# Kernel tuning notes

Hardware: AMD Instinct MI355X
Metric: run time of the kernel (lower is better)

## Reference

```python
import jax, jax.numpy as jnp
import numpy as np
from jax import lax

B, N, D = 16, 2048, 256
H = 64  # hidden_dim
EPS = 1e-5


def zero_softmax(x, eps=EPS):
    # zeros stay exactly zero: exp(0)-1 == 0
    e = jnp.exp(x) - 1.0
    return e / (jnp.sum(e, axis=-1, keepdims=True) + eps)


def setup_inputs() -> dict:
    key = jax.random.key(0)
    ks = jax.random.split(key, 9)
    s_in = 1.0 / np.sqrt(D)
    x = jax.random.normal(ks[0], (B, N, D), dtype=jnp.float32)
    Wq = jax.random.uniform(ks[1], (D, H), jnp.float32, -s_in, s_in)
    bq = jax.random.uniform(ks[2], (H,), jnp.float32, -s_in, s_in)
    Wk = jax.random.uniform(ks[3], (D, H), jnp.float32, -s_in, s_in)
    bk = jax.random.uniform(ks[4], (H,), jnp.float32, -s_in, s_in)
    Wv = jax.random.uniform(ks[5], (D, H), jnp.float32, -s_in, s_in)
    bv = jax.random.uniform(ks[6], (H,), jnp.float32, -s_in, s_in)
    s_c = 1.0 / 3.0  # conv fan_in = 1*3*3 = 9
    conv_w = jax.random.uniform(ks[7], (1, 1, 3, 3), jnp.float32, -s_c, s_c)
    conv_b = jax.random.uniform(ks[8], (1,), jnp.float32, -s_c, s_c)
    return {"x": x, "Wq": Wq, "bq": bq, "Wk": Wk, "bk": bk,
            "Wv": Wv, "bv": bv, "conv_w": conv_w, "conv_b": conv_b}


def reference(x, Wq, bq, Wk, bk, Wv, bv, conv_w, conv_b):
    scale = H ** (-0.5)
    q = jnp.einsum('bnd,dh->bnh', x, Wq) + bq
    k = jnp.einsum('bnd,dh->bnh', x, Wk) + bk
    v = jnp.einsum('bnd,dh->bnh', x, Wv) + bv
    A_dense = jnp.einsum('bnh,bmh->bnm', q, k) * scale  # [B, N, N]
    A_in = A_dense[:, None, :, :]  # [B, 1, N, N]
    A_conv = lax.conv_general_dilated(
        A_in, conv_w, window_strides=(1, 1), padding='SAME',
        dimension_numbers=('NCHW', 'OIHW', 'NCHW')) + conv_b[None, :, None, None]
    A_conv = jax.nn.sigmoid(A_conv)[:, 0, :, :]
    A_sparse = jax.nn.relu(A_dense - A_conv)
    A_norm = zero_softmax(A_sparse)
    return jnp.einsum('bnm,bmh->bnh', A_norm, v)
```

## Files before the change

kernel.cpp:

```cpp
#include <hip/hip_runtime.h>
#include <hip/hip_bf16.h>

typedef __bf16 bf16_t;
typedef __bf16 bf16x8 __attribute__((ext_vector_type(8)));
typedef float  floatx4 __attribute__((ext_vector_type(4)));

#define BQ 16
#define NTOK 2048
#define DIM 256
#define HD 64

__global__ __launch_bounds__(256) void k_prep(const float* __restrict__ Wq,
                                              const float* __restrict__ Wk,
                                              const float* __restrict__ Wv,
                                              bf16_t* __restrict__ wt,
                                              float* __restrict__ outz,
                                              float* __restrict__ rsz) {
    int o = blockIdx.x * 256 + threadIdx.x;
    if (o < 49152) {
        int w = o >> 14;
        int r = o & 16383;
        int h = r >> 8;
        int d = r & 255;
        const float* W = (w == 0) ? Wq : ((w == 1) ? Wk : Wv);
        wt[o] = (bf16_t)W[d * 64 + h];
    }
    float4 z = make_float4(0.f, 0.f, 0.f, 0.f);
    for (int u = o; u < 532480; u += 262144) {
        if (u < 524288) ((float4*)outz)[u] = z;
        else            ((float4*)rsz)[u - 524288] = z;
    }
}

#define XS 264
__global__ __launch_bounds__(256) void k_qkv(const float* __restrict__ x,
                                             const bf16_t* __restrict__ wt,
                                             const float* __restrict__ bq,
                                             const float* __restrict__ bk,
                                             const float* __restrict__ bv,
                                             bf16_t* __restrict__ qb,
                                             bf16_t* __restrict__ kb,
                                             bf16_t* __restrict__ vt) {
    __shared__ bf16_t x_ls[64 * XS];
    __shared__ bf16_t vt_ls[64 * 72];

    int b  = blockIdx.x >> 5;
    int t0 = (blockIdx.x & 31) << 6;
    int t  = threadIdx.x;
    int lane = t & 63;
    int w    = t >> 6;
    int m_   = lane & 15;
    int q4   = lane >> 4;

    const bf16_t* wrow = wt + (16 * w + m_) * 256 + q4 * 8;

    bf16x8 bfr[2][3];
    #pragma unroll
    for (int wi = 0; wi < 3; ++wi)
        bfr[0][wi] = *(const bf16x8*)(wrow + wi * 16384);

    for (int tau = t; tau < 4096; tau += 256) {
        int row = tau >> 6, ch = tau & 63;
        float4 v = ((const float4*)x)[(size_t)(b * NTOK + t0 + row) * 64 + ch];
        bf16_t tmp[4] = {(bf16_t)v.x, (bf16_t)v.y, (bf16_t)v.z, (bf16_t)v.w};
        *(uint2*)(&x_ls[row * XS + ch * 4]) = *(uint2*)tmp;
    }
    __syncthreads();

    floatx4 acc[3][4];
    #pragma unroll
    for (int wi = 0; wi < 3; ++wi)
        #pragma unroll
        for (int mt = 0; mt < 4; ++mt) acc[wi][mt] = floatx4{0.f, 0.f, 0.f, 0.f};

    #pragma unroll
    for (int ks = 0; ks < 8; ++ks) {
        if (ks < 7) {
            #pragma unroll
            for (int wi = 0; wi < 3; ++wi)
                bfr[(ks + 1) & 1][wi] = *(const bf16x8*)(wrow + wi * 16384 + (ks + 1) * 32);
        }
        #pragma unroll
        for (int mt = 0; mt < 4; ++mt) {
            bf16x8 afrag = *(const bf16x8*)(&x_ls[(16 * mt + m_) * XS + ks * 32 + q4 * 8]);
            #pragma unroll
            for (int wi = 0; wi < 3; ++wi)
                acc[wi][mt] = __builtin_amdgcn_mfma_f32_16x16x32_bf16(afrag, bfr[ks & 1][wi], acc[wi][mt], 0, 0, 0);
        }
    }

    float biasq = bq[16 * w + m_];
    float biask = bk[16 * w + m_];
    float biasv = bv[16 * w + m_];

    #pragma unroll
    for (int mt = 0; mt < 4; ++mt)
        #pragma unroll
        for (int r = 0; r < 4; ++r) {
            int tok = t0 + 16 * mt + 4 * q4 + r;
            qb[(size_t)(b * NTOK + tok) * 64 + 16 * w + m_] = (bf16_t)((acc[0][mt][r] + biasq) * 0.125f);
            kb[(size_t)(b * NTOK + tok) * 64 + 16 * w + m_] = (bf16_t)(acc[1][mt][r] + biask);
            vt_ls[(16 * w + m_) * 72 + 16 * mt + 4 * q4 + r] = (bf16_t)(acc[2][mt][r] + biasv);
        }
    __syncthreads();
    for (int tau = t; tau < 512; tau += 256) {
        int h = tau >> 3, ch = tau & 7;
        uint4 val = *(const uint4*)(&vt_ls[h * 72 + ch * 8]);
        *(uint4*)(vt + (size_t)(b * 64 + h) * NTOK + t0 + ch * 8) = val;
    }
}

#define SP 72
#define RINT 62
#define L2E 1.44269504f

static __device__ __forceinline__ bf16x8 as_bf16x8(uint4 u) {
    union { uint4 a; bf16x8 b; } c; c.a = u; return c.b;
}

__global__ __launch_bounds__(512, 3) void k_attn(const bf16_t* __restrict__ qb,
                                                 const bf16_t* __restrict__ kb,
                                                 const bf16_t* __restrict__ vt,
                                                 const float* __restrict__ conv_w,
                                                 const float* __restrict__ conv_b,
                                                 float* __restrict__ outp,
                                                 float* __restrict__ rsg) {
    __shared__ bf16_t k_ls[64 * SP];
    __shared__ bf16_t v_ls[64 * SP];
    __shared__ bf16_t a_bf[64 * SP];
    __shared__ bf16_t p_raw[64 * SP + 8];
    bf16_t* pv_ls = p_raw + 8;

    int b  = blockIdx.z;
    int r0 = blockIdx.x * RINT;
    int cy = blockIdx.y;
    int it_beg = (cy * 34) / 3;
    int it_end = ((cy + 1) * 34) / 3;

    int t = threadIdx.x, lane = t & 63, w = t >> 6;
    int m_ = lane & 15, q4 = lane >> 4;
    int wtj = w & 3;
    int wti = (w >> 2) << 1;

    const uint* vt32 = (const uint*)vt + (size_t)b * 64 * 1024;
    const bf16_t* kb_b = kb + (size_t)b * NTOK * 64;

    int krow = t >> 3, kch = t & 7;

    uint4 kreg;
    uint  vreg[4];
    auto load_k = [&](int c0) {
        int g = c0 - 1 + krow;
        uint4 val = make_uint4(0u, 0u, 0u, 0u);
        if (g >= 0 && g < NTOK)
            val = *(const uint4*)(kb_b + (size_t)g * 64 + kch * 8);
        kreg = val;
    };
    auto load_v = [&](int c0) {
        int cb2 = (c0 >> 1) + 4 * kch;
        #pragma unroll
        for (int j = 0; j < 4; ++j) {
            uint val = 0u;
            if (cb2 + j < 1024) val = vt32[krow * 1024 + cb2 + j];
            vreg[j] = val;
        }
    };

    load_k(it_beg * RINT);
    load_v(it_beg * RINT);

    float cw9[9];
    #pragma unroll
    for (int i = 0; i < 9; ++i) cw9[i] = conv_w[i] * L2E;
    float cbv2 = conv_b[0] * L2E;
    int koff = ((wtj & 1) << 3) + ((wtj & 2) * 12);
    bf16x8 bK[3];
    #pragma unroll
    for (int di = 0; di < 3; ++di) {
        bf16_t tmp[8];
        #pragma unroll
        for (int jj = 0; jj < 8; ++jj) {
            int d = koff + q4 * 8 + jj - (16 * wtj + m_) + 1;
            tmp[jj] = (bf16_t)((d >= 0 && d < 3) ? cw9[3 * di + d] : 0.f);
        }
        bK[di] = *(bf16x8*)tmp;
    }

    bf16x8 qreg[2][2];
    #pragma unroll
    for (int p = 0; p < 2; ++p) {
        int g = r0 - 1 + 16 * (wti + p) + m_;
        #pragma unroll
        for (int ks = 0; ks < 2; ++ks) {
            uint4 val = make_uint4(0u, 0u, 0u, 0u);
            if (g >= 0 && g < NTOK)
                val = *(const uint4*)(qb + (size_t)(b * NTOK + g) * 64 + ks * 32 + q4 * 8);
            qreg[p][ks] = as_bf16x8(val);
        }
    }

    for (int u = t; u < 2308; u += 512) ((uint*)p_raw)[u] = 0u;

    *(uint4*)(&k_ls[krow * SP + kch * 8]) = kreg;
    load_k((it_beg + 1) * RINT);

    floatx4 accO[2], rsacc[2];
    accO[0] = floatx4{0.f, 0.f, 0.f, 0.f};
    accO[1] = floatx4{0.f, 0.f, 0.f, 0.f};
    rsacc[0] = floatx4{0.f, 0.f, 0.f, 0.f};
    rsacc[1] = floatx4{0.f, 0.f, 0.f, 0.f};

    float mj = ((wtj == 0 && m_ == 0) || (wtj == 3 && m_ == 15)) ? 0.f : 1.f;
    int jm1 = 16 * wtj + m_ - 1;

    __syncthreads();

    for (int itg = it_beg; itg < it_end; ++itg) {
        floatx4 areg[2];
        {
            bf16x8 bfr0 = *(const bf16x8*)(&k_ls[(16 * wtj + m_) * SP + q4 * 8]);
            bf16x8 bfr1 = *(const bf16x8*)(&k_ls[(16 * wtj + m_) * SP + 32 + q4 * 8]);
            #pragma unroll
            for (int p = 0; p < 2; ++p) {
                floatx4 a = floatx4{0.f, 0.f, 0.f, 0.f};
                a = __builtin_amdgcn_mfma_f32_16x16x32_bf16(qreg[p][0], bfr0, a, 0, 0, 0);
                a = __builtin_amdgcn_mfma_f32_16x16x32_bf16(qreg[p][1], bfr1, a, 0, 0, 0);
                areg[p] = a;
                int rbase = 16 * (wti + p) + 4 * q4;
                #pragma unroll
                for (int r = 0; r < 4; ++r)
                    a_bf[(rbase + r) * SP + 16 * wtj + m_] = (bf16_t)a[r];
            }
        }
        __syncthreads();

        *(uint4*)(&k_ls[krow * SP + kch * 8]) = kreg;
        *(uint4*)(&v_ls[krow * SP + 8 * kch]) = make_uint4(vreg[0], vreg[1], vreg[2], vreg[3]);
        load_k((itg + 2) * RINT);
        load_v((itg + 1) * RINT);

        #pragma unroll
        for (int p = 0; p < 2; ++p) {
            int arow = 16 * (wti + p) + m_ - 1;
            floatx4 c = floatx4{cbv2, cbv2, cbv2, cbv2};
            #pragma unroll
            for (int di = 0; di < 3; ++di) {
                bf16x8 af = *(const bf16x8*)(&a_bf[((arow + di) & 63) * SP + koff + q4 * 8]);
                c = __builtin_amdgcn_mfma_f32_16x16x32_bf16(af, bK[di], c, 0, 0, 0);
            }
            int rbase = 16 * (wti + p) + 4 * q4;
            #pragma unroll
            for (int r = 0; r < 4; ++r) {
                float sig = __builtin_amdgcn_rcpf(1.f + __builtin_amdgcn_exp2f(-c[r]));
                float s = fmaxf(areg[p][r] - sig, 0.f);
                float ev = (__builtin_amdgcn_exp2f(s * L2E) - 1.f) * mj;
                if (p == 0 && r == 0) { if (wti == 0) ev = (q4 == 0) ? 0.f : ev; }
                if (p == 1 && r == 3) { if (wti == 2) ev = (q4 == 3) ? 0.f : ev; }
                rsacc[p][r] += ev;
                pv_ls[(rbase + r) * SP + jm1] = (bf16_t)ev;
            }
        }
        __syncthreads();

        #pragma unroll
        for (int ks = 0; ks < 2; ++ks) {
            bf16x8 bfr = *(const bf16x8*)(&v_ls[(16 * wtj + m_) * SP + ks * 32 + q4 * 8]);
            #pragma unroll
            for (int p = 0; p < 2; ++p) {
                bf16x8 af = *(const bf16x8*)(&pv_ls[(16 * (wti + p) + m_) * SP + ks * 32 + q4 * 8]);
                accO[p] = __builtin_amdgcn_mfma_f32_16x16x32_bf16(af, bfr, accO[p], 0, 0, 0);
            }
        }
    }

    #pragma unroll
    for (int p = 0; p < 2; ++p)
        #pragma unroll
        for (int r = 0; r < 4; ++r) {
            float s = rsacc[p][r];
            s += __shfl_xor(s, 1);
            s += __shfl_xor(s, 2);
            s += __shfl_xor(s, 4);
            s += __shfl_xor(s, 8);
            if (m_ == 0) {
                int grow = r0 + 16 * (wti + p) + 4 * q4 + r - 1;
                if ((unsigned)grow < NTOK) atomicAdd(&rsg[b * NTOK + grow], s);
            }
        }

    #pragma unroll
    for (int p = 0; p < 2; ++p) {
        int rbase = 16 * (wti + p) + 4 * q4;
        #pragma unroll
        for (int r = 0; r < 4; ++r) {
            int i = rbase + r;
            int grow = r0 + i - 1;
            if (i >= 1 && i < 63 && grow < NTOK)
                atomicAdd(&outp[((size_t)(b * NTOK + grow) << 6) + 16 * wtj + m_], accO[p][r]);
        }
    }
}

__global__ __launch_bounds__(256) void k_norm(float* __restrict__ out,
                                              const float* __restrict__ rsg) {
    int gid = blockIdx.x * 256 + threadIdx.x;
    float4 o = ((float4*)out)[gid];
    float d = rsg[gid >> 4] + 1e-5f;
    float inv = 1.f / d;
    o.x *= inv; o.y *= inv; o.z *= inv; o.w *= inv;
    ((float4*)out)[gid] = o;
}

extern "C" void kernel_launch(void* const* d_in, const int* in_sizes, int n_in,
                              void* d_out, int out_size, void* d_ws, size_t ws_size,
                              hipStream_t stream) {
    const float* x  = (const float*)d_in[0];
    const float* Wq = (const float*)d_in[1];
    const float* bq = (const float*)d_in[2];
    const float* Wk = (const float*)d_in[3];
    const float* bk = (const float*)d_in[4];
    const float* Wv = (const float*)d_in[5];
    const float* bv = (const float*)d_in[6];
    const float* cw = (const float*)d_in[7];
    const float* cb = (const float*)d_in[8];
    float* out = (float*)d_out;

    char* ws = (char*)d_ws;
    bf16_t* wt = (bf16_t*)ws;
    bf16_t* qb = (bf16_t*)(ws + 98304);
    bf16_t* kb = (bf16_t*)(ws + 98304 + 4194304);
    bf16_t* vt = (bf16_t*)(ws + 98304 + 8388608);
    float*  rsg = (float*)(ws + 98304 + 12582912);

    k_prep<<<dim3(1024), dim3(256), 0, stream>>>(Wq, Wk, Wv, wt, out, rsg);
    k_qkv<<<dim3(512), dim3(256), 0, stream>>>(x, wt, bq, bk, bv, qb, kb, vt);
    k_attn<<<dim3(34, 3, BQ), dim3(512), 0, stream>>>(qb, kb, vt, cw, cb, out, rsg);
    k_norm<<<dim3(2048), dim3(256), 0, stream>>>(out, rsg);
}
```

Measured before the change: 204.1 us.

## Swizzle LDS score tiles and fold log2e scaling into Q and sigmoid

Applies an XOR swizzle to the byte offsets of the A-score and P tiles in shared memory, meant to remove LDS bank conflicts on the scattered bf16 writes and the vector reads. Masked rim entries are redirected to a spare slot in the padded row rather than being multiplied by zero before the store. The log2(e) factor is folded into the Q scaling and into the conv bias so the exp2 paths need fewer multiplies. This changes the numerical form of the sigmoid: conv weights in bf16 are no longer prescaled, and a ln2 constant compensates in the denominator. The swizzle pattern must exactly match between writes and reads.

```diff
diff --git a/kernel.cpp b/kernel.cpp
--- a/kernel.cpp
+++ b/kernel.cpp
@@ -98,7 +98,7 @@
         #pragma unroll
         for (int r = 0; r < 4; ++r) {
             int tok = t0 + 16 * mt + 4 * q4 + r;
-            qb[(size_t)(b * NTOK + tok) * 64 + 16 * w + m_] = (bf16_t)((acc[0][mt][r] + biasq) * 0.125f);
+            qb[(size_t)(b * NTOK + tok) * 64 + 16 * w + m_] = (bf16_t)((acc[0][mt][r] + biasq) * 0.18033688f);
             kb[(size_t)(b * NTOK + tok) * 64 + 16 * w + m_] = (bf16_t)(acc[1][mt][r] + biask);
             vt_ls[(16 * w + m_) * 72 + 16 * mt + 4 * q4 + r] = (bf16_t)(acc[2][mt][r] + biasv);
         }
@@ -128,8 +128,7 @@
     __shared__ bf16_t k_ls[64 * SP];
     __shared__ bf16_t v_ls[64 * SP];
     __shared__ bf16_t a_bf[64 * SP];
-    __shared__ bf16_t p_raw[64 * SP + 8];
-    bf16_t* pv_ls = p_raw + 8;
+    __shared__ bf16_t p_ls[64 * SP];
 
     int b  = blockIdx.z;
     int r0 = blockIdx.x * RINT;
@@ -169,10 +168,6 @@
     load_k(it_beg * RINT);
     load_v(it_beg * RINT);
 
-    float cw9[9];
-    #pragma unroll
-    for (int i = 0; i < 9; ++i) cw9[i] = conv_w[i] * L2E;
-    float cbv2 = conv_b[0] * L2E;
     int koff = ((wtj & 1) << 3) + ((wtj & 2) * 12);
     bf16x8 bK[3];
     #pragma unroll
@@ -181,10 +176,11 @@
         #pragma unroll
         for (int jj = 0; jj < 8; ++jj) {
             int d = koff + q4 * 8 + jj - (16 * wtj + m_) + 1;
-            tmp[jj] = (bf16_t)((d >= 0 && d < 3) ? cw9[3 * di + d] : 0.f);
+            tmp[jj] = (bf16_t)((d >= 0 && d < 3) ? conv_w[3 * di + d] : 0.f);
         }
         bK[di] = *(bf16x8*)tmp;
     }
+    float cbv2 = conv_b[0] * L2E + 0.52876637f;
 
     bf16x8 qreg[2][2];
     #pragma unroll
@@ -199,7 +195,7 @@
         }
     }
 
-    for (int u = t; u < 2308; u += 512) ((uint*)p_raw)[u] = 0u;
+    for (int u = t; u < 2304; u += 512) ((uint*)p_ls)[u] = 0u;
 
     *(uint4*)(&k_ls[krow * SP + kch * 8]) = kreg;
     load_k((it_beg + 1) * RINT);
@@ -210,8 +206,18 @@
     rsacc[0] = floatx4{0.f, 0.f, 0.f, 0.f};
     rsacc[1] = floatx4{0.f, 0.f, 0.f, 0.f};
 
-    float mj = ((wtj == 0 && m_ == 0) || (wtj == 3 && m_ == 15)) ? 0.f : 1.f;
+    bool rimL = (wtj == 0 && m_ == 0) || (wtj == 3 && m_ == 15);
     int jm1 = 16 * wtj + m_ - 1;
+    int pb  = rimL ? 128 : ((2 * jm1) ^ (q4 << 4));
+    int pbA = (wti == 0 && q4 == 0) ? 136 : pb;
+    int pbB = (wti == 2 && q4 == 3) ? 136 : pb;
+    float mj = rimL ? 0.f : 1.f;
+    float mA = (wti == 0 && q4 == 0) ? 0.f : mj;
+    float mB = (wti == 2 && q4 == 3) ? 0.f : mj;
+
+    int abyte = (32 * wtj + 2 * m_) ^ (q4 << 4);
+    int cb_   = 2 * koff + q4 * 16;
+    int pswz  = (m_ >> 2) << 4;
 
     __syncthreads();
 
@@ -229,7 +235,7 @@
                 int rbase = 16 * (wti + p) + 4 * q4;
                 #pragma unroll
                 for (int r = 0; r < 4; ++r)
-                    a_bf[(rbase + r) * SP + 16 * wtj + m_] = (bf16_t)a[r];
+                    *(bf16_t*)((char*)a_bf + (rbase + r) * 144 + abyte) = (bf16_t)a[r];
             }
         }
         __syncthreads();
@@ -245,19 +251,21 @@
             floatx4 c = floatx4{cbv2, cbv2, cbv2, cbv2};
             #pragma unroll
             for (int di = 0; di < 3; ++di) {
-                bf16x8 af = *(const bf16x8*)(&a_bf[((arow + di) & 63) * SP + koff + q4 * 8]);
+                int rr = (arow + di) & 63;
+                bf16x8 af = *(const bf16x8*)((const char*)a_bf + rr * 144 + (cb_ ^ (((rr >> 2) & 3) << 4)));
                 c = __builtin_amdgcn_mfma_f32_16x16x32_bf16(af, bK[di], c, 0, 0, 0);
             }
             int rbase = 16 * (wti + p) + 4 * q4;
             #pragma unroll
             for (int r = 0; r < 4; ++r) {
-                float sig = __builtin_amdgcn_rcpf(1.f + __builtin_amdgcn_exp2f(-c[r]));
-                float s = fmaxf(areg[p][r] - sig, 0.f);
-                float ev = (__builtin_amdgcn_exp2f(s * L2E) - 1.f) * mj;
-                if (p == 0 && r == 0) { if (wti == 0) ev = (q4 == 0) ? 0.f : ev; }
-                if (p == 1 && r == 3) { if (wti == 2) ev = (q4 == 3) ? 0.f : ev; }
-                rsacc[p][r] += ev;
-                pv_ls[(rbase + r) * SP + jm1] = (bf16_t)ev;
+                float e  = __builtin_amdgcn_exp2f(-c[r]);
+                float sg = __builtin_amdgcn_rcpf(e + 0.69314718f);
+                float s  = fmaxf(areg[p][r] - sg, 0.f);
+                float ev = __builtin_amdgcn_exp2f(s) - 1.f;
+                float mk  = (p == 0 && r == 0) ? mA : ((p == 1 && r == 3) ? mB : mj);
+                int   pb_ = (p == 0 && r == 0) ? pbA : ((p == 1 && r == 3) ? pbB : pb);
+                rsacc[p][r] += ev * mk;
+                *(bf16_t*)((char*)p_ls + (rbase + r) * 144 + pb_) = (bf16_t)ev;
             }
         }
         __syncthreads();
@@ -267,7 +275,8 @@
             bf16x8 bfr = *(const bf16x8*)(&v_ls[(16 * wtj + m_) * SP + ks * 32 + q4 * 8]);
             #pragma unroll
             for (int p = 0; p < 2; ++p) {
-                bf16x8 af = *(const bf16x8*)(&pv_ls[(16 * (wti + p) + m_) * SP + ks * 32 + q4 * 8]);
+                bf16x8 af = *(const bf16x8*)((const char*)p_ls + (16 * (wti + p) + m_) * 144
+                                             + ((ks * 64 + q4 * 16) ^ pswz));
                 accO[p] = __builtin_amdgcn_mfma_f32_16x16x32_bf16(af, bfr, accO[p], 0, 0, 0);
             }
         }
```

Result: slower. 224.7 us (+10.1%).
